# Kernel tuning notes

Measured on AMD Instinct MI355X. Metric: run time of the kernel, lower is better.

## Reference

```python
import jax, jax.numpy as jnp
import numpy as np

B, T, D, H = 64, 512, 1024, 1024


def setup_inputs() -> dict:
    key = jax.random.key(0)
    ks = jax.random.split(key, 9)
    s_in = 1.0 / np.sqrt(D + H)  # torch Linear default init scale
    inp = {
        "x": jax.random.normal(ks[0], (B, T, D), dtype=jnp.float32),
        "Wi": jax.random.uniform(ks[1], (H, D + H), jnp.float32, -s_in, s_in),
        "bi": jax.random.uniform(ks[2], (H,), jnp.float32, -s_in, s_in),
        "Wf": jax.random.uniform(ks[3], (H, D + H), jnp.float32, -s_in, s_in),
        "bf": jax.random.uniform(ks[4], (H,), jnp.float32, -s_in, s_in),
        "Wo": jax.random.uniform(ks[5], (H, D + H), jnp.float32, -s_in, s_in),
        "bo": jax.random.uniform(ks[6], (H,), jnp.float32, -s_in, s_in),
        "Wc": jax.random.uniform(ks[7], (H, D + H), jnp.float32, -s_in, s_in),
        "bc": jax.random.uniform(ks[8], (H,), jnp.float32, -s_in, s_in),
    }
    return inp


def reference(x, Wi, bi, Wf, bf, Wo, bo, Wc, bc):
    # x: [B, T, D]; returns stacked hidden states [T, B, H]
    batch = x.shape[0]
    hidden = Wi.shape[0]
    h0 = jnp.zeros((batch, hidden), dtype=x.dtype)
    c0 = jnp.zeros((batch, hidden), dtype=x.dtype)

    def step(carry, x_t):
        h, c = carry
        inp = jnp.concatenate([x_t, h], axis=1)  # [B, D+H]
        f = jax.nn.sigmoid(inp @ Wf.T + bf)
        i = jax.nn.sigmoid(inp @ Wi.T + bi)
        o = jax.nn.sigmoid(inp @ Wo.T + bo)
        g = jnp.tanh(inp @ Wc.T + bc)
        c_new = f * c + i * g
        h_new = o * jnp.tanh(c_new)
        return (h_new, c_new), h_new

    xs = jnp.transpose(x, (1, 0, 2))  # [T, B, D]
    _, h_states = jax.lax.scan(step, (h0, c0), xs)
    return h_states  # [T, B, H]
```

## Files before the change

### kernel.cpp

```cpp
#include <hip/hip_runtime.h>


typedef short short8 __attribute__((ext_vector_type(8)));
typedef float f32x4 __attribute__((ext_vector_type(4)));

#define NBLK 128
#define TPB 256

__device__ __forceinline__ unsigned bfbits(float f) {
  unsigned u = __float_as_uint(f);
  return ((u + 0x7fffu + ((u >> 16) & 1u)) >> 16) & 0xffffu;
}

__device__ __forceinline__ short8 cvt8(const float* p) {
  const float4* q = (const float4*)p;
  float4 a = q[0], b = q[1];
  short8 r;
  r[0] = (short)bfbits(a.x); r[1] = (short)bfbits(a.y);
  r[2] = (short)bfbits(a.z); r[3] = (short)bfbits(a.w);
  r[4] = (short)bfbits(b.x); r[5] = (short)bfbits(b.y);
  r[6] = (short)bfbits(b.z); r[7] = (short)bfbits(b.w);
  return r;
}

__device__ __forceinline__ float sigmoidf_(float x) {
  return 1.0f / (1.0f + __expf(-x));
}
__device__ __forceinline__ float tanhf_(float x) {
  float ax = fabsf(x);
  float e = __expf(-2.0f * ax);
  float r = (1.0f - e) / (1.0f + e);
  return copysignf(r, x);
}

__global__ void cvt_x_kernel(const float* __restrict__ x,
                             unsigned short* __restrict__ xb, int n4) {
  int i = blockIdx.x * blockDim.x + threadIdx.x;
  int stride = gridDim.x * blockDim.x;
  const float4* xv = (const float4*)x;
  uint2* ov = (uint2*)xb;
  for (; i < n4; i += stride) {
    float4 v = xv[i];
    uint2 o;
    o.x = bfbits(v.x) | (bfbits(v.y) << 16);
    o.y = bfbits(v.z) | (bfbits(v.w) << 16);
    ov[i] = o;
  }
}

__global__ __launch_bounds__(TPB, 1) void lstm_persist(
    const float* __restrict__ x, const unsigned short* __restrict__ xb,
    const float* __restrict__ Wi, const float* __restrict__ Wf,
    const float* __restrict__ Wo, const float* __restrict__ Wc,
    const float* __restrict__ bi, const float* __restrict__ bfv,
    const float* __restrict__ bo, const float* __restrict__ bc,
    unsigned short* __restrict__ hist, unsigned* __restrict__ flags,
    float* __restrict__ out) {
  constexpr int B = 64, T = 512, D = 1024, H = 1024;
  const int tid = threadIdx.x;
  const int bid = blockIdx.x;
  const int lane = tid & 63;
  const int w = tid >> 6;
  const int cl = lane & 15;
  const int kg = lane >> 4;
  const int j0 = bid * 8;

  __builtin_amdgcn_fence(__ATOMIC_ACQUIRE, "agent");

  __shared__ float part[4][32][68];

  const float* Wg[4] = {Wi, Wf, Wo, Wc};
  short8 bxw[2][8], bhw[2][8];
#pragma unroll
  for (int nt = 0; nt < 2; ++nt) {
    int g = 2 * nt + (cl >> 3);
    const float* wrow = Wg[g] + (size_t)(j0 + (cl & 7)) * 2048;
#pragma unroll
    for (int kf = 0; kf < 8; ++kf) {
      int kx = 256 * w + 32 * kf + 8 * kg;
      bxw[nt][kf] = cvt8(wrow + kx);
      bhw[nt][kf] = cvt8(wrow + 1024 + kx);
    }
  }

  const int row = tid >> 2;
  const int up = tid & 3;
  float biasv[4][2];
#pragma unroll
  for (int k = 0; k < 2; ++k) {
    biasv[0][k] = bi[j0 + 2 * up + k];
    biasv[1][k] = bfv[j0 + 2 * up + k];
    biasv[2][k] = bo[j0 + 2 * up + k];
    biasv[3][k] = bc[j0 + 2 * up + k];
  }
  float cst[2] = {0.0f, 0.0f};

  const int kxbase = 256 * w + 8 * kg;

  unsigned* hz = (unsigned*)hist;
  __hip_atomic_store(&hz[bid * TPB + tid], 0u, __ATOMIC_RELAXED,
                     __HIP_MEMORY_SCOPE_AGENT);
  __syncthreads();
  if (tid == 0)
    __hip_atomic_store(&flags[bid * 32], 1u, __ATOMIC_RELAXED,
                       __HIP_MEMORY_SCOPE_AGENT);

  for (int t = 0; t < T; ++t) {
    const unsigned short* hprev = hist + (size_t)t * 65536;
    unsigned short* hnext = hist + (size_t)(t + 1) * 65536;

    f32x4 acc[4][2];
#pragma unroll
    for (int mt = 0; mt < 4; ++mt)
#pragma unroll
      for (int nt = 0; nt < 2; ++nt) acc[mt][nt] = (f32x4)0.0f;

#pragma unroll
    for (int kf = 0; kf < 8; ++kf) {
      int kx = kxbase + 32 * kf;
      short8 af[4];
      if (xb) {
#pragma unroll
        for (int mt = 0; mt < 4; ++mt) {
          int b = 16 * mt + cl;
          af[mt] = *(const short8*)(xb + ((size_t)b * T + t) * D + kx);
        }
      } else {
#pragma unroll
        for (int mt = 0; mt < 4; ++mt) {
          int b = 16 * mt + cl;
          af[mt] = cvt8(x + ((size_t)b * T + t) * D + kx);
        }
      }
#pragma unroll
      for (int mt = 0; mt < 4; ++mt) {
        acc[mt][0] = __builtin_amdgcn_mfma_f32_16x16x32_bf16(
            af[mt], bxw[0][kf], acc[mt][0], 0, 0, 0);
        acc[mt][1] = __builtin_amdgcn_mfma_f32_16x16x32_bf16(
            af[mt], bxw[1][kf], acc[mt][1], 0, 0, 0);
      }
    }

    {
      const unsigned target = (unsigned)(t + 1);
      const unsigned* fp = flags + (size_t)(32 * w + (lane & 31)) * 32;
      while (true) {
        unsigned v =
            __hip_atomic_load(fp, __ATOMIC_RELAXED, __HIP_MEMORY_SCOPE_AGENT);
        if (__all((int)(v >= target))) break;
        __builtin_amdgcn_s_sleep(1);
      }
    }
    asm volatile("" ::: "memory");

    short8 ah[8][4];
#pragma unroll
    for (int kf = 0; kf < 8; ++kf) {
      int kh = kxbase + 32 * kf;
#pragma unroll
      for (int mt = 0; mt < 4; ++mt)
        ah[kf][mt] = *(const short8*)(hprev + (size_t)(16 * mt + cl) * H + kh);
    }
#pragma unroll
    for (int kf = 0; kf < 8; ++kf) {
#pragma unroll
      for (int mt = 0; mt < 4; ++mt) {
        acc[mt][0] = __builtin_amdgcn_mfma_f32_16x16x32_bf16(
            ah[kf][mt], bhw[0][kf], acc[mt][0], 0, 0, 0);
        acc[mt][1] = __builtin_amdgcn_mfma_f32_16x16x32_bf16(
            ah[kf][mt], bhw[1][kf], acc[mt][1], 0, 0, 0);
      }
    }

#pragma unroll
    for (int mt = 0; mt < 4; ++mt)
#pragma unroll
      for (int nt = 0; nt < 2; ++nt)
        *(f32x4*)&part[w][16 * nt + cl][16 * mt + 4 * kg] = acc[mt][nt];
    __syncthreads();

    float hv[2];
#pragma unroll
    for (int k = 0; k < 2; ++k) {
      int u = 2 * up + k;
      float pre[4];
#pragma unroll
      for (int g = 0; g < 4; ++g) {
        float s = biasv[g][k];
#pragma unroll
        for (int ww = 0; ww < 4; ++ww) s += part[ww][8 * g + u][row];
        pre[g] = s;
      }
      float iv = sigmoidf_(pre[0]);
      float fv = sigmoidf_(pre[1]);
      float ov = sigmoidf_(pre[2]);
      float gv = tanhf_(pre[3]);
      cst[k] = fv * cst[k] + iv * gv;
      hv[k] = ov * tanhf_(cst[k]);
    }
    unsigned hpack = bfbits(hv[0]) | (bfbits(hv[1]) << 16);
    __hip_atomic_store((unsigned*)(hnext + (size_t)row * H + j0 + 2 * up),
                       hpack, __ATOMIC_RELAXED, __HIP_MEMORY_SCOPE_AGENT);

    __syncthreads();
    asm volatile("" ::: "memory");
    if (tid == 0)
      __hip_atomic_store(&flags[bid * 32], (unsigned)(t + 2), __ATOMIC_RELAXED,
                         __HIP_MEMORY_SCOPE_AGENT);

    float* op = out + ((size_t)t * B + row) * H + j0 + 2 * up;
    __builtin_nontemporal_store(hv[0], op);
    __builtin_nontemporal_store(hv[1], op + 1);
  }
}

extern "C" void kernel_launch(void* const* d_in, const int* in_sizes, int n_in,
                              void* d_out, int out_size, void* d_ws,
                              size_t ws_size, hipStream_t stream) {
  const float* x = (const float*)d_in[0];
  const float* Wi = (const float*)d_in[1];
  const float* bi = (const float*)d_in[2];
  const float* Wf = (const float*)d_in[3];
  const float* bfv = (const float*)d_in[4];
  const float* Wo = (const float*)d_in[5];
  const float* bo = (const float*)d_in[6];
  const float* Wc = (const float*)d_in[7];
  const float* bc = (const float*)d_in[8];
  float* out = (float*)d_out;

  char* ws = (char*)d_ws;
  const size_t xb_bytes = (size_t)64 * 512 * 1024 * 2;
  const size_t hist_bytes = (size_t)513 * 64 * 1024 * 2;
  const size_t fl_bytes = (size_t)NBLK * 32 * 4;

  unsigned short* xb = nullptr;
  size_t off = 0;
  if (ws_size >= xb_bytes + hist_bytes + fl_bytes) {
    xb = (unsigned short*)ws;
    off = xb_bytes;
  }
  unsigned short* hist = (unsigned short*)(ws + off);
  off += hist_bytes;
  unsigned* flags = (unsigned*)(ws + off);

  hipMemsetAsync(flags, 0, fl_bytes, stream);
  if (xb) cvt_x_kernel<<<2048, 256, 0, stream>>>(x, xb, (64 * 512 * 1024) / 4);
  lstm_persist<<<NBLK, TPB, 0, stream>>>(x, xb, Wi, Wf, Wo, Wc, bi, bfv, bo, bc,
                                         hist, flags, out);
}
```

Baseline: 4.507 ms.

## Halve persistent grid to 64 blocks of 512 threads, fewer flags to poll

Restructures the persistent LSTM so each block owns 16 hidden units with 8 waves (two gate-column groups by four K-slices) instead of 8 units with 4 waves. This halves the number of blocks that must signal and be polled in the per-step grid barrier, and each wave now polls 16 flags. It also drops the s_sleep in the spin loop, hoists the x/h pointer arithmetic out of the time loop, removes the fp32 fallback path, and replaces nontemporal output stores with plain stores. The costs are fewer CUs in use, larger dynamic LDS, and busier spinning.

Result: slower. 8.184 ms (+81.6%).

```diff
diff --git a/kernel.cpp b/kernel.cpp
--- a/kernel.cpp
+++ b/kernel.cpp
@@ -4,8 +4,8 @@
 typedef short short8 __attribute__((ext_vector_type(8)));
 typedef float f32x4 __attribute__((ext_vector_type(4)));
 
-#define NBLK 128
-#define TPB 256
+#define NBLK 64
+#define TPB 512
 
 __device__ __forceinline__ unsigned bfbits(float f) {
   unsigned u = __float_as_uint(f);
@@ -48,7 +48,9 @@
   }
 }
 
-__global__ __launch_bounds__(TPB, 1) void lstm_persist(
+#define PART(G, kw, col, row) part[((((G)*4 + (kw)) * 32 + (col)) * 68) + (row)]
+
+__global__ __launch_bounds__(TPB, 2) void lstm_persist(
     const float* __restrict__ x, const unsigned short* __restrict__ xb,
     const float* __restrict__ Wi, const float* __restrict__ Wf,
     const float* __restrict__ Wo, const float* __restrict__ Wc,
@@ -61,30 +63,32 @@
   const int bid = blockIdx.x;
   const int lane = tid & 63;
   const int w = tid >> 6;
+  const int G = w >> 2;
+  const int kw = w & 3;
   const int cl = lane & 15;
   const int kg = lane >> 4;
-  const int j0 = bid * 8;
+  const int j0 = bid * 16;
 
   __builtin_amdgcn_fence(__ATOMIC_ACQUIRE, "agent");
 
-  __shared__ float part[4][32][68];
+  extern __shared__ float part[];
 
   const float* Wg[4] = {Wi, Wf, Wo, Wc};
   short8 bxw[2][8], bhw[2][8];
 #pragma unroll
   for (int nt = 0; nt < 2; ++nt) {
     int g = 2 * nt + (cl >> 3);
-    const float* wrow = Wg[g] + (size_t)(j0 + (cl & 7)) * 2048;
-#pragma unroll
-    for (int kf = 0; kf < 8; ++kf) {
-      int kx = 256 * w + 32 * kf + 8 * kg;
+    const float* wrow = Wg[g] + (size_t)(j0 + 8 * G + (cl & 7)) * 2048;
+#pragma unroll
+    for (int kf = 0; kf < 8; ++kf) {
+      int kx = 256 * kw + 32 * kf + 8 * kg;
       bxw[nt][kf] = cvt8(wrow + kx);
       bhw[nt][kf] = cvt8(wrow + 1024 + kx);
     }
   }
 
-  const int row = tid >> 2;
-  const int up = tid & 3;
+  const int row = tid >> 3;
+  const int up = tid & 7;
   float biasv[4][2];
 #pragma unroll
   for (int k = 0; k < 2; ++k) {
@@ -95,7 +99,16 @@
   }
   float cst[2] = {0.0f, 0.0f};
 
-  const int kxbase = 256 * w + 8 * kg;
+  const int kxbase = 256 * kw + 8 * kg;
+
+  const unsigned short* pxb[4];
+#pragma unroll
+  for (int mt = 0; mt < 4; ++mt)
+    pxb[mt] = xb + (size_t)(16 * mt + cl) * T * D + kxbase;
+  int hoff[4];
+#pragma unroll
+  for (int mt = 0; mt < 4; ++mt) hoff[mt] = (16 * mt + cl) * H + kxbase;
+  float* pout = out + (size_t)row * H + j0 + 2 * up;
 
   unsigned* hz = (unsigned*)hist;
   __hip_atomic_store(&hz[bid * TPB + tid], 0u, __ATOMIC_RELAXED,
@@ -117,21 +130,10 @@
 
 #pragma unroll
     for (int kf = 0; kf < 8; ++kf) {
-      int kx = kxbase + 32 * kf;
       short8 af[4];
-      if (xb) {
-#pragma unroll
-        for (int mt = 0; mt < 4; ++mt) {
-          int b = 16 * mt + cl;
-          af[mt] = *(const short8*)(xb + ((size_t)b * T + t) * D + kx);
-        }
-      } else {
-#pragma unroll
-        for (int mt = 0; mt < 4; ++mt) {
-          int b = 16 * mt + cl;
-          af[mt] = cvt8(x + ((size_t)b * T + t) * D + kx);
-        }
-      }
+#pragma unroll
+      for (int mt = 0; mt < 4; ++mt)
+        af[mt] = *(const short8*)(pxb[mt] + 32 * kf);
 #pragma unroll
       for (int mt = 0; mt < 4; ++mt) {
         acc[mt][0] = __builtin_amdgcn_mfma_f32_16x16x32_bf16(
@@ -140,15 +142,16 @@
             af[mt], bxw[1][kf], acc[mt][1], 0, 0, 0);
       }
     }
+#pragma unroll
+    for (int mt = 0; mt < 4; ++mt) pxb[mt] += D;
 
     {
       const unsigned target = (unsigned)(t + 1);
-      const unsigned* fp = flags + (size_t)(32 * w + (lane & 31)) * 32;
+      const unsigned* fp = flags + (size_t)(16 * kw + (lane & 15)) * 32;
       while (true) {
         unsigned v =
             __hip_atomic_load(fp, __ATOMIC_RELAXED, __HIP_MEMORY_SCOPE_AGENT);
         if (__all((int)(v >= target))) break;
-        __builtin_amdgcn_s_sleep(1);
       }
     }
     asm volatile("" ::: "memory");
@@ -156,10 +159,9 @@
     short8 ah[8][4];
 #pragma unroll
     for (int kf = 0; kf < 8; ++kf) {
-      int kh = kxbase + 32 * kf;
 #pragma unroll
       for (int mt = 0; mt < 4; ++mt)
-        ah[kf][mt] = *(const short8*)(hprev + (size_t)(16 * mt + cl) * H + kh);
+        ah[kf][mt] = *(const short8*)(hprev + hoff[mt] + 32 * kf);
     }
 #pragma unroll
     for (int kf = 0; kf < 8; ++kf) {
@@ -176,19 +178,21 @@
     for (int mt = 0; mt < 4; ++mt)
 #pragma unroll
       for (int nt = 0; nt < 2; ++nt)
-        *(f32x4*)&part[w][16 * nt + cl][16 * mt + 4 * kg] = acc[mt][nt];
+        *(f32x4*)&PART(G, kw, 16 * nt + cl, 16 * mt + 4 * kg) = acc[mt][nt];
     __syncthreads();
 
     float hv[2];
 #pragma unroll
     for (int k = 0; k < 2; ++k) {
       int u = 2 * up + k;
+      int uG = u >> 3;
+      int uc = u & 7;
       float pre[4];
 #pragma unroll
       for (int g = 0; g < 4; ++g) {
         float s = biasv[g][k];
 #pragma unroll
-        for (int ww = 0; ww < 4; ++ww) s += part[ww][8 * g + u][row];
+        for (int ww = 0; ww < 4; ++ww) s += PART(uG, ww, 8 * g + uc, row);
         pre[g] = s;
       }
       float iv = sigmoidf_(pre[0]);
@@ -208,9 +212,9 @@
       __hip_atomic_store(&flags[bid * 32], (unsigned)(t + 2), __ATOMIC_RELAXED,
                          __HIP_MEMORY_SCOPE_AGENT);
 
-    float* op = out + ((size_t)t * B + row) * H + j0 + 2 * up;
-    __builtin_nontemporal_store(hv[0], op);
-    __builtin_nontemporal_store(hv[1], op + 1);
+    pout[0] = hv[0];
+    pout[1] = hv[1];
+    pout += (size_t)B * H;
   }
 }
 
@@ -233,18 +237,14 @@
   const size_t hist_bytes = (size_t)513 * 64 * 1024 * 2;
   const size_t fl_bytes = (size_t)NBLK * 32 * 4;
 
-  unsigned short* xb = nullptr;
-  size_t off = 0;
-  if (ws_size >= xb_bytes + hist_bytes + fl_bytes) {
-    xb = (unsigned short*)ws;
-    off = xb_bytes;
-  }
+  unsigned short* xb = (unsigned short*)ws;
+  size_t off = xb_bytes;
   unsigned short* hist = (unsigned short*)(ws + off);
   off += hist_bytes;
   unsigned* flags = (unsigned*)(ws + off);
 
   hipMemsetAsync(flags, 0, fl_bytes, stream);
-  if (xb) cvt_x_kernel<<<2048, 256, 0, stream>>>(x, xb, (64 * 512 * 1024) / 4);
-  lstm_persist<<<NBLK, TPB, 0, stream>>>(x, xb, Wi, Wf, Wo, Wc, bi, bfv, bo, bc,
-                                         hist, flags, out);
-}
+  cvt_x_kernel<<<2048, 256, 0, stream>>>(x, xb, (64 * 512 * 1024) / 4);
+  lstm_persist<<<NBLK, TPB, 69632, stream>>>(x, xb, Wi, Wf, Wo, Wc, bi, bfv,
+                                             bo, bc, hist, flags, out);
+}
```
